# Optimization experiments

Measured on AMD Instinct MI355X. Metric: run time of the kernel, lower is better.

## Reference

```python
import jax, jax.numpy as jnp
import numpy as np

N_NODES = 100000
N_EDGES = 3200000
D_IN = 128
D_HID = 128
D_FF = 256
N_CLASSES = 26
N_GRAPHS = 512


def setup_inputs() -> dict:
    key = jax.random.key(0)
    ks = jax.random.split(key, 12)
    s = 0.05
    return {
        "x": jax.random.normal(ks[0], (N_NODES, D_IN), dtype=jnp.float32),
        "edge_index": jax.random.randint(ks[1], (2, N_EDGES), 0, N_NODES, dtype=jnp.int64),
        "batch": jnp.sort(jax.random.randint(ks[2], (N_NODES,), 0, N_GRAPHS, dtype=jnp.int64)),
        "W1": jax.random.normal(ks[3], (D_IN, D_HID), dtype=jnp.float32) * s,
        "b1": jnp.zeros((D_HID,), dtype=jnp.float32),
        "W2": jax.random.normal(ks[4], (D_HID, D_HID), dtype=jnp.float32) * s,
        "b2": jnp.zeros((D_HID,), dtype=jnp.float32),
        "W3": jax.random.normal(ks[5], (D_HID, D_HID), dtype=jnp.float32) * s,
        "b3": jnp.zeros((D_HID,), dtype=jnp.float32),
        "Wfc": jax.random.normal(ks[6], (D_HID, D_FF), dtype=jnp.float32) * s,
        "bfc": jnp.zeros((D_FF,), dtype=jnp.float32),
        "Wfc2": jax.random.normal(ks[7], (D_FF, N_CLASSES), dtype=jnp.float32) * s,
        "bfc2": jnp.zeros((N_CLASSES,), dtype=jnp.float32),
    }


def _gcn_layer(x, src, dst, norm, W, b):
    # GCNConv: h = x @ W; out[dst] += norm_e * h[src]; out += b
    h = x @ W                                   # [N, D]
    msg = h[src] * norm[:, None]                # [E+N, D] gather + scale
    agg = jax.ops.segment_sum(msg, dst, num_segments=N_NODES)
    return agg + b


def reference(x, edge_index, batch, W1, b1, W2, b2, W3, b3, Wfc, bfc, Wfc2, bfc2):
    # add self-loops (PyG GCNConv default) and compute symmetric normalization once
    loop = jnp.arange(N_NODES, dtype=edge_index.dtype)
    src = jnp.concatenate([edge_index[0], loop])
    dst = jnp.concatenate([edge_index[1], loop])
    deg = jax.ops.segment_sum(jnp.ones_like(dst, dtype=x.dtype), dst, num_segments=N_NODES)
    dinv = jnp.where(deg > 0, jax.lax.rsqrt(deg), 0.0)
    norm = dinv[src] * dinv[dst]               # D^{-1/2} A_hat D^{-1/2}

    h = jax.nn.relu(_gcn_layer(x, src, dst, norm, W1, b1))
    h = jax.nn.relu(_gcn_layer(h, src, dst, norm, W2, b2))
    h = jax.nn.relu(_gcn_layer(h, src, dst, norm, W3, b3))

    # global mean pool over graphs
    sums = jax.ops.segment_sum(h, batch, num_segments=N_GRAPHS)       # [G, D]
    cnts = jax.ops.segment_sum(jnp.ones((h.shape[0],), h.dtype), batch, num_segments=N_GRAPHS)
    pooled = sums / jnp.maximum(cnts, 1.0)[:, None]

    out = jax.nn.relu(pooled @ Wfc + bfc)       # dropout is identity at inference
    return out @ Wfc2 + bfc2                    # [G, num_classes]
```

## Files before the change

kernel.cpp:

```cpp
#include <hip/hip_runtime.h>
#include <hip/hip_bf16.h>

typedef __bf16 bf16;
typedef __attribute__((ext_vector_type(8))) __bf16 bf16x8;
typedef __attribute__((ext_vector_type(4))) float f32x4;

constexpr int N_NODES   = 100000;
constexpr int N_PAD     = 100032;
constexpr int D         = 128;
constexpr int D_FF      = 256;
constexpr int N_CLASSES = 26;
constexpr int N_GRAPHS  = 512;
constexpr int NB1       = 256;
constexpr int NBUCK     = (N_NODES + 511) / 512;

__device__ inline float2 bf2f(unsigned u) {
    float lo = __uint_as_float(u << 16);
    float hi = __uint_as_float(u & 0xffff0000u);
    return make_float2(lo, hi);
}


__global__ __launch_bounds__(1024) void p1_hist(const int* __restrict__ edst,
                                                int* __restrict__ gcount, int e) {
    __shared__ int cnt[NBUCK];
    for (int t = threadIdx.x; t < NBUCK; t += 1024) cnt[t] = 0;
    __syncthreads();
    int chunk = (e + NB1 - 1) / NB1;
    int lo = blockIdx.x * chunk;
    int hi = min(e, lo + chunk);
    for (int i = lo + threadIdx.x; i < hi; i += 1024)
        atomicAdd(&cnt[edst[i] >> 9], 1);
    __syncthreads();
    for (int t = threadIdx.x; t < NBUCK; t += 1024)
        gcount[t * NB1 + blockIdx.x] = cnt[t];
}

__global__ __launch_bounds__(256) void scan1(const int* __restrict__ in,
                                             int* out, int* bsum, int n) {
    __shared__ int sd[256];
    int i = blockIdx.x * 256 + threadIdx.x;
    int v = (i < n) ? in[i] : 0;
    sd[threadIdx.x] = v; __syncthreads();
    for (int off = 1; off < 256; off <<= 1) {
        int t = (threadIdx.x >= off) ? sd[threadIdx.x - off] : 0;
        __syncthreads();
        sd[threadIdx.x] += t;
        __syncthreads();
    }
    if (i < n) out[i] = sd[threadIdx.x] - v;
    if (threadIdx.x == 255) bsum[blockIdx.x] = sd[255];
}

__global__ __launch_bounds__(1024) void misc_kernel(const int* __restrict__ bsum,
                                                    int* __restrict__ boff, int nb,
                                                    const int* __restrict__ batch,
                                                    int* __restrict__ starts, int n,
                                                    const float* __restrict__ W0,
                                                    const float* __restrict__ W1,
                                                    const float* __restrict__ W2,
                                                    bf16* __restrict__ WT3) {
    int t = threadIdx.x;
    if (blockIdx.x == 0) {
        if (t <= N_GRAPHS) {
            int lo = 0, hi = n;
            while (lo < hi) {
                int mid = (lo + hi) >> 1;
                if (batch[mid] < t) lo = mid + 1; else hi = mid;
            }
            starts[t] = lo;
        }
        __shared__ int sd[1024];
        int v = (t < nb) ? bsum[t] : 0;
        sd[t] = v; __syncthreads();
        for (int off = 1; off < 1024; off <<= 1) {
            int x = (t >= off) ? sd[t - off] : 0;
            __syncthreads();
            sd[t] += x;
            __syncthreads();
        }
        if (t < nb) boff[t] = sd[t] - v;
    } else {
        int idx = (blockIdx.x - 1) * 1024 + t;
        int l = idx >> 14;
        int rem = idx & 16383;
        int nn = rem >> 7;
        int kk = rem & 127;
        const float* W = (l == 0) ? W0 : (l == 1) ? W1 : W2;
        WT3[idx] = (bf16)W[kk * D + nn];
    }
}

__global__ __launch_bounds__(1024) void p3_scatter(const int* __restrict__ esrc,
                                                   const int* __restrict__ edst,
                                                   const int* __restrict__ gbase,
                                                   const int* __restrict__ boff,
                                                   int* __restrict__ ebuf, int e) {
    __shared__ int cur[NBUCK];
    for (int t = threadIdx.x; t < NBUCK; t += 1024)
        cur[t] = gbase[t * NB1 + blockIdx.x] + boff[t];
    __syncthreads();
    int chunk = (e + NB1 - 1) / NB1;
    int lo = blockIdx.x * chunk;
    int hi = min(e, lo + chunk);
    for (int i = lo + threadIdx.x; i < hi; i += 1024) {
        int d = edst[i], s = esrc[i];
        int pos = atomicAdd(&cur[d >> 9], 1);
        ebuf[pos] = (s << 9) | (d & 511);
    }
}

__global__ __launch_bounds__(1024) void p45_fill(const int* __restrict__ ebuf,
                                                 const int* __restrict__ gbase,
                                                 const int* __restrict__ boff,
                                                 float* __restrict__ dinv,
                                                 int* __restrict__ rowptr,
                                                 int* __restrict__ csrc, int e, int n) {
    __shared__ int cnt[512];
    __shared__ int ps[512];
    __shared__ int cur[512];
    int b = blockIdx.x, t = threadIdx.x;
    if (t < 512) cnt[t] = 0;
    __syncthreads();
    int lo = gbase[b * NB1] + boff[b];
    int hi = (b + 1 < NBUCK) ? gbase[(b + 1) * NB1] + boff[b + 1] : e;
    for (int i = lo + t; i < hi; i += 1024)
        atomicAdd(&cnt[ebuf[i] & 511], 1);
    __syncthreads();
    int a = (t < 512) ? cnt[t] : 0;
    if (t < 512) ps[t] = a;
    __syncthreads();
    for (int off = 1; off < 512; off <<= 1) {
        int v = (t >= off && t < 512) ? ps[t - off] : 0;
        __syncthreads();
        if (t < 512) ps[t] += v;
        __syncthreads();
    }
    if (t < 512) {
        int g0 = lo + ps[t] - a;
        int node = b * 512 + t;
        cur[t] = g0;
        if (node < n) {
            rowptr[node] = g0;
            dinv[node] = 1.0f / sqrtf((float)(a + 1));
        }
    }
    if (b == 0 && t == 0) rowptr[n] = e;
    __syncthreads();
    for (int i = lo + t; i < hi; i += 1024) {
        int pe = ebuf[i];
        int pos = atomicAdd(&cur[pe & 511], 1);
        csrc[pos] = pe >> 9;
    }
}


__global__ __launch_bounds__(256) void gemm_kernel(const bf16* __restrict__ A,
                                                   const bf16* __restrict__ WT,
                                                   bf16* __restrict__ C,
                                                   const float* __restrict__ dinv, int n) {
    int wave = threadIdx.x >> 6;
    int lane = threadIdx.x & 63;
    int m16  = lane & 15;
    int quad = lane >> 4;
    int row0 = blockIdx.x * 64 + wave * 16;

    bf16x8 a[4];
    const bf16* arow = A + (row0 + m16) * D + quad * 8;
#pragma unroll
    for (int kt = 0; kt < 4; ++kt)
        a[kt] = *(const bf16x8*)(arow + kt * 32);

    float sc[4];
#pragma unroll
    for (int r = 0; r < 4; ++r) {
        int rr = row0 + quad * 4 + r;
        sc[r] = (rr < n) ? dinv[rr] : 0.f;
    }

#pragma unroll
    for (int nt = 0; nt < 8; ++nt) {
        f32x4 acc = {0.f, 0.f, 0.f, 0.f};
        const bf16* brow = WT + (nt * 16 + m16) * D + quad * 8;
#pragma unroll
        for (int kt = 0; kt < 4; ++kt) {
            bf16x8 b = *(const bf16x8*)(brow + kt * 32);
            acc = __builtin_amdgcn_mfma_f32_16x16x32_bf16(a[kt], b, acc, 0, 0, 0);
        }
#pragma unroll
        for (int r = 0; r < 4; ++r)
            C[(row0 + quad * 4 + r) * D + nt * 16 + m16] = (bf16)(sc[r] * acc[r]);
    }
}

__global__ __launch_bounds__(256) void gemm_f32_kernel(const float* __restrict__ A,
                                                       const bf16* __restrict__ WT,
                                                       bf16* __restrict__ C,
                                                       const float* __restrict__ dinv, int n) {
    int wave = threadIdx.x >> 6;
    int lane = threadIdx.x & 63;
    int m16  = lane & 15;
    int quad = lane >> 4;
    int row0 = blockIdx.x * 64 + wave * 16;
    int arowi = row0 + m16;

    bf16x8 a[4];
    const float* arow = A + (size_t)arowi * D + quad * 8;
#pragma unroll
    for (int kt = 0; kt < 4; ++kt) {
        float4 f0 = make_float4(0.f, 0.f, 0.f, 0.f);
        float4 f1 = make_float4(0.f, 0.f, 0.f, 0.f);
        if (arowi < n) {
            f0 = *(const float4*)(arow + kt * 32);
            f1 = *(const float4*)(arow + kt * 32 + 4);
        }
        bf16x8 v = { (bf16)f0.x, (bf16)f0.y, (bf16)f0.z, (bf16)f0.w,
                     (bf16)f1.x, (bf16)f1.y, (bf16)f1.z, (bf16)f1.w };
        a[kt] = v;
    }

    float sc[4];
#pragma unroll
    for (int r = 0; r < 4; ++r) {
        int rr = row0 + quad * 4 + r;
        sc[r] = (rr < n) ? dinv[rr] : 0.f;
    }

#pragma unroll
    for (int nt = 0; nt < 8; ++nt) {
        f32x4 acc = {0.f, 0.f, 0.f, 0.f};
        const bf16* brow = WT + (nt * 16 + m16) * D + quad * 8;
#pragma unroll
        for (int kt = 0; kt < 4; ++kt) {
            bf16x8 b = *(const bf16x8*)(brow + kt * 32);
            acc = __builtin_amdgcn_mfma_f32_16x16x32_bf16(a[kt], b, acc, 0, 0, 0);
        }
#pragma unroll
        for (int r = 0; r < 4; ++r)
            C[(row0 + quad * 4 + r) * D + nt * 16 + m16] = (bf16)(sc[r] * acc[r]);
    }
}

__global__ __launch_bounds__(256) void spmm_kernel(const bf16* __restrict__ h,
                                                   const int* __restrict__ rowptr,
                                                   const int* __restrict__ csrc,
                                                   const float* __restrict__ dinv,
                                                   const float* __restrict__ bias,
                                                   bf16* __restrict__ out, int n) {
    int v = blockIdx.x * 4 + (threadIdx.x >> 6);
    if (v >= n) return;
    int lane = threadIdx.x & 63;
    int g = lane >> 4;
    int c = lane & 15;
    int s = rowptr[v], e = rowptr[v + 1];
    float dv = dinv[v];

    float acc[8] = {0.f, 0.f, 0.f, 0.f, 0.f, 0.f, 0.f, 0.f};

    if (g == 0) {
        uint4 u = *(const uint4*)(h + (size_t)v * D + c * 8);
        float2 f0 = bf2f(u.x), f1 = bf2f(u.y), f2 = bf2f(u.z), f3 = bf2f(u.w);
        acc[0] = f0.x; acc[1] = f0.y; acc[2] = f1.x; acc[3] = f1.y;
        acc[4] = f2.x; acc[5] = f2.y; acc[6] = f3.x; acc[7] = f3.y;
    }

    int j = s + g;
    for (; j + 12 < e; j += 16) {
        int s0 = csrc[j], s1 = csrc[j + 4], s2 = csrc[j + 8], s3 = csrc[j + 12];
        uint4 u0 = *(const uint4*)(h + (size_t)s0 * D + c * 8);
        uint4 u1 = *(const uint4*)(h + (size_t)s1 * D + c * 8);
        uint4 u2 = *(const uint4*)(h + (size_t)s2 * D + c * 8);
        uint4 u3 = *(const uint4*)(h + (size_t)s3 * D + c * 8);
        {
            float2 a0 = bf2f(u0.x), a1 = bf2f(u0.y), a2 = bf2f(u0.z), a3 = bf2f(u0.w);
            acc[0] += a0.x; acc[1] += a0.y; acc[2] += a1.x; acc[3] += a1.y;
            acc[4] += a2.x; acc[5] += a2.y; acc[6] += a3.x; acc[7] += a3.y;
        }
        {
            float2 a0 = bf2f(u1.x), a1 = bf2f(u1.y), a2 = bf2f(u1.z), a3 = bf2f(u1.w);
            acc[0] += a0.x; acc[1] += a0.y; acc[2] += a1.x; acc[3] += a1.y;
            acc[4] += a2.x; acc[5] += a2.y; acc[6] += a3.x; acc[7] += a3.y;
        }
        {
            float2 a0 = bf2f(u2.x), a1 = bf2f(u2.y), a2 = bf2f(u2.z), a3 = bf2f(u2.w);
            acc[0] += a0.x; acc[1] += a0.y; acc[2] += a1.x; acc[3] += a1.y;
            acc[4] += a2.x; acc[5] += a2.y; acc[6] += a3.x; acc[7] += a3.y;
        }
        {
            float2 a0 = bf2f(u3.x), a1 = bf2f(u3.y), a2 = bf2f(u3.z), a3 = bf2f(u3.w);
            acc[0] += a0.x; acc[1] += a0.y; acc[2] += a1.x; acc[3] += a1.y;
            acc[4] += a2.x; acc[5] += a2.y; acc[6] += a3.x; acc[7] += a3.y;
        }
    }
    for (; j < e; j += 4) {
        int s0 = csrc[j];
        uint4 u0 = *(const uint4*)(h + (size_t)s0 * D + c * 8);
        float2 a0 = bf2f(u0.x), a1 = bf2f(u0.y), a2 = bf2f(u0.z), a3 = bf2f(u0.w);
        acc[0] += a0.x; acc[1] += a0.y; acc[2] += a1.x; acc[3] += a1.y;
        acc[4] += a2.x; acc[5] += a2.y; acc[6] += a3.x; acc[7] += a3.y;
    }

#pragma unroll
    for (int d = 0; d < 8; ++d) {
        acc[d] += __shfl_xor(acc[d], 16);
        acc[d] += __shfl_xor(acc[d], 32);
    }

    if (g == 0) {
        float4 bi0 = *(const float4*)(bias + c * 8);
        float4 bi1 = *(const float4*)(bias + c * 8 + 4);
        bf16x8 o;
        o[0] = (bf16)fmaxf(fmaf(dv, acc[0], bi0.x), 0.f);
        o[1] = (bf16)fmaxf(fmaf(dv, acc[1], bi0.y), 0.f);
        o[2] = (bf16)fmaxf(fmaf(dv, acc[2], bi0.z), 0.f);
        o[3] = (bf16)fmaxf(fmaf(dv, acc[3], bi0.w), 0.f);
        o[4] = (bf16)fmaxf(fmaf(dv, acc[4], bi1.x), 0.f);
        o[5] = (bf16)fmaxf(fmaf(dv, acc[5], bi1.y), 0.f);
        o[6] = (bf16)fmaxf(fmaf(dv, acc[6], bi1.z), 0.f);
        o[7] = (bf16)fmaxf(fmaf(dv, acc[7], bi1.w), 0.f);
        *(bf16x8*)(out + v * D + c * 8) = o;
    }
}

__global__ __launch_bounds__(256) void poolfc_kernel(const bf16* __restrict__ h,
                                                     const int* __restrict__ starts,
                                                     const float* __restrict__ Wfc,
                                                     const float* __restrict__ bfc,
                                                     const float* __restrict__ Wfc2,
                                                     const float* __restrict__ bfc2,
                                                     float* __restrict__ out) {
    __shared__ float part[3][D];
    __shared__ float pr[D];
    __shared__ float hid[D_FF];
    __shared__ float red[N_CLASSES][9];
    int g = blockIdx.x;
    int w = threadIdx.x >> 6, lane = threadIdx.x & 63;
    int s = starts[g], e = starts[g + 1];
    float ax = 0.f, ay = 0.f;
    for (int r = s + w; r < e; r += 4) {
        unsigned u = *(const unsigned*)(h + r * D + lane * 2);
        float2 f = bf2f(u);
        ax += f.x; ay += f.y;
    }
    if (w > 0) { part[w - 1][lane * 2] = ax; part[w - 1][lane * 2 + 1] = ay; }
    __syncthreads();
    if (w == 0) {
#pragma unroll
        for (int k = 0; k < 3; ++k) { ax += part[k][lane * 2]; ay += part[k][lane * 2 + 1]; }
        float c = fmaxf((float)(e - s), 1.0f);
        pr[lane * 2]     = ax / c;
        pr[lane * 2 + 1] = ay / c;
    }
    __syncthreads();
    int t = threadIdx.x;
    float a0 = 0.f, a1 = 0.f, a2 = 0.f, a3 = 0.f;
    for (int k = 0; k < D; k += 4) {
        a0 = fmaf(pr[k],     Wfc[k * D_FF + t],       a0);
        a1 = fmaf(pr[k + 1], Wfc[(k + 1) * D_FF + t], a1);
        a2 = fmaf(pr[k + 2], Wfc[(k + 2) * D_FF + t], a2);
        a3 = fmaf(pr[k + 3], Wfc[(k + 3) * D_FF + t], a3);
    }
    hid[t] = fmaxf((a0 + a1) + (a2 + a3) + bfc[t], 0.f);
    __syncthreads();
    if (t < N_CLASSES * 8) {
        int cls = t >> 3, kk = t & 7;
        float o = 0.f;
        for (int k = kk; k < D_FF; k += 8)
            o = fmaf(hid[k], Wfc2[k * N_CLASSES + cls], o);
        red[cls][kk] = o;
    }
    __syncthreads();
    if (t < N_CLASSES) {
        float o = bfc2[t];
#pragma unroll
        for (int k = 0; k < 8; ++k) o += red[t][k];
        out[g * N_CLASSES + t] = o;
    }
}


extern "C" void kernel_launch(void* const* d_in, const int* in_sizes, int n_in,
                              void* d_out, int out_size, void* d_ws, size_t ws_size,
                              hipStream_t stream) {
    const float* x     = (const float*)d_in[0];
    const int*   eidx  = (const int*)d_in[1];
    const int*   batch = (const int*)d_in[2];
    const float* W[3]  = { (const float*)d_in[3], (const float*)d_in[5], (const float*)d_in[7] };
    const float* b[3]  = { (const float*)d_in[4], (const float*)d_in[6], (const float*)d_in[8] };
    const float* Wfc   = (const float*)d_in[9];
    const float* bfc   = (const float*)d_in[10];
    const float* Wfc2  = (const float*)d_in[11];
    const float* bfc2  = (const float*)d_in[12];
    float* out = (float*)d_out;

    const int E = in_sizes[1] / 2;
    const int N = in_sizes[0] / D;
    const int* esrc = eidx;
    const int* edst = eidx + E;

    uint8_t* base = (uint8_t*)d_ws;
    size_t off = 0;
    auto alloc = [&](size_t bytes) -> void* {
        void* p = base + off;
        off = (off + bytes + 255) & ~(size_t)255;
        return p;
    };
    bf16*  hA     = (bf16*) alloc((size_t)N_PAD * D * 2);
    bf16*  hB     = (bf16*) alloc((size_t)N_PAD * D * 2);
    bf16*  WT3    = (bf16*) alloc((size_t)3 * D * D * 2);
    int*   csrc   = (int*)  alloc((size_t)E * 4);
    int*   ebuf   = (int*)  alloc((size_t)E * 4);
    int*   gcount = (int*)  alloc((size_t)NBUCK * NB1 * 4);
    int*   gbase  = (int*)  alloc((size_t)(NBUCK * NB1 + 1) * 4);
    int*   rowptr = (int*)  alloc((size_t)(N + 1) * 4);
    float* dinv   = (float*)alloc((size_t)N * 4);
    int*   bsum   = (int*)  alloc(4096);
    int*   boff   = (int*)  alloc(4096);
    int*   starts = (int*)  alloc((size_t)(N_GRAPHS + 1) * 4);
    (void)ws_size; (void)n_in; (void)out_size;

    const int GB  = N_PAD / 64;
    const int SB  = (N + 3) / 4;
    const int GCN = NBUCK * NB1;
    const int GCB = (GCN + 255) / 256;

    p1_hist<<<NB1, 1024, 0, stream>>>(edst, gcount, E);
    scan1<<<GCB, 256, 0, stream>>>(gcount, gbase, bsum, GCN);
    misc_kernel<<<49, 1024, 0, stream>>>(bsum, boff, GCB, batch, starts, N,
                                         W[0], W[1], W[2], WT3);
    p3_scatter<<<NB1, 1024, 0, stream>>>(esrc, edst, gbase, boff, ebuf, E);
    p45_fill<<<NBUCK, 1024, 0, stream>>>(ebuf, gbase, boff, dinv, rowptr, csrc, E, N);

    gemm_f32_kernel<<<GB, 256, 0, stream>>>(x, WT3, hA, dinv, N);
    spmm_kernel<<<SB, 256, 0, stream>>>(hA, rowptr, csrc, dinv, b[0], hB, N);
    for (int l = 1; l < 3; ++l) {
        gemm_kernel<<<GB, 256, 0, stream>>>(hB, WT3 + (size_t)l * D * D, hA, dinv, N);
        spmm_kernel<<<SB, 256, 0, stream>>>(hA, rowptr, csrc, dinv, b[l], hB, N);
    }

    poolfc_kernel<<<N_GRAPHS, 256, 0, stream>>>(hB, starts, Wfc, bfc, Wfc2, bfc2, out);
}
```

Baseline: 632.4 us.

## Fuse SpMM aggregation with next-layer GEMM through shared memory tile

```diff
diff --git a/kernel.cpp b/kernel.cpp
--- a/kernel.cpp
+++ b/kernel.cpp
@@ -155,44 +155,6 @@
 }
 
 
-__global__ __launch_bounds__(256) void gemm_kernel(const bf16* __restrict__ A,
-                                                   const bf16* __restrict__ WT,
-                                                   bf16* __restrict__ C,
-                                                   const float* __restrict__ dinv, int n) {
-    int wave = threadIdx.x >> 6;
-    int lane = threadIdx.x & 63;
-    int m16  = lane & 15;
-    int quad = lane >> 4;
-    int row0 = blockIdx.x * 64 + wave * 16;
-
-    bf16x8 a[4];
-    const bf16* arow = A + (row0 + m16) * D + quad * 8;
-#pragma unroll
-    for (int kt = 0; kt < 4; ++kt)
-        a[kt] = *(const bf16x8*)(arow + kt * 32);
-
-    float sc[4];
-#pragma unroll
-    for (int r = 0; r < 4; ++r) {
-        int rr = row0 + quad * 4 + r;
-        sc[r] = (rr < n) ? dinv[rr] : 0.f;
-    }
-
-#pragma unroll
-    for (int nt = 0; nt < 8; ++nt) {
-        f32x4 acc = {0.f, 0.f, 0.f, 0.f};
-        const bf16* brow = WT + (nt * 16 + m16) * D + quad * 8;
-#pragma unroll
-        for (int kt = 0; kt < 4; ++kt) {
-            bf16x8 b = *(const bf16x8*)(brow + kt * 32);
-            acc = __builtin_amdgcn_mfma_f32_16x16x32_bf16(a[kt], b, acc, 0, 0, 0);
-        }
-#pragma unroll
-        for (int r = 0; r < 4; ++r)
-            C[(row0 + quad * 4 + r) * D + nt * 16 + m16] = (bf16)(sc[r] * acc[r]);
-    }
-}
-
 __global__ __launch_bounds__(256) void gemm_f32_kernel(const float* __restrict__ A,
                                                        const bf16* __restrict__ WT,
                                                        bf16* __restrict__ C,
@@ -241,32 +203,25 @@
     }
 }
 
-__global__ __launch_bounds__(256) void spmm_kernel(const bf16* __restrict__ h,
-                                                   const int* __restrict__ rowptr,
-                                                   const int* __restrict__ csrc,
-                                                   const float* __restrict__ dinv,
-                                                   const float* __restrict__ bias,
-                                                   bf16* __restrict__ out, int n) {
-    int v = blockIdx.x * 4 + (threadIdx.x >> 6);
-    if (v >= n) return;
-    int lane = threadIdx.x & 63;
-    int g = lane >> 4;
-    int c = lane & 15;
-    int s = rowptr[v], e = rowptr[v + 1];
-    float dv = dinv[v];
-
-    float acc[8] = {0.f, 0.f, 0.f, 0.f, 0.f, 0.f, 0.f, 0.f};
-
-    if (g == 0) {
+__device__ inline void agg_node(const bf16* __restrict__ h, int v, int n, int c,
+                                const int* __restrict__ rowptr,
+                                const int* __restrict__ csrc,
+                                const float* __restrict__ dinv,
+                                float& dv, float acc[8]) {
+    int s = 0, e = 0;
+    dv = 0.f;
+    if (v < n) { s = rowptr[v]; e = rowptr[v + 1]; dv = dinv[v]; }
+#pragma unroll
+    for (int d = 0; d < 8; ++d) acc[d] = 0.f;
+    if (v < n) {
         uint4 u = *(const uint4*)(h + (size_t)v * D + c * 8);
         float2 f0 = bf2f(u.x), f1 = bf2f(u.y), f2 = bf2f(u.z), f3 = bf2f(u.w);
         acc[0] = f0.x; acc[1] = f0.y; acc[2] = f1.x; acc[3] = f1.y;
         acc[4] = f2.x; acc[5] = f2.y; acc[6] = f3.x; acc[7] = f3.y;
     }
-
-    int j = s + g;
-    for (; j + 12 < e; j += 16) {
-        int s0 = csrc[j], s1 = csrc[j + 4], s2 = csrc[j + 8], s3 = csrc[j + 12];
+    int j = s;
+    for (; j + 3 < e; j += 4) {
+        int s0 = csrc[j], s1 = csrc[j + 1], s2 = csrc[j + 2], s3 = csrc[j + 3];
         uint4 u0 = *(const uint4*)(h + (size_t)s0 * D + c * 8);
         uint4 u1 = *(const uint4*)(h + (size_t)s1 * D + c * 8);
         uint4 u2 = *(const uint4*)(h + (size_t)s2 * D + c * 8);
@@ -292,34 +247,93 @@
             acc[4] += a2.x; acc[5] += a2.y; acc[6] += a3.x; acc[7] += a3.y;
         }
     }
-    for (; j < e; j += 4) {
+    for (; j < e; ++j) {
         int s0 = csrc[j];
         uint4 u0 = *(const uint4*)(h + (size_t)s0 * D + c * 8);
         float2 a0 = bf2f(u0.x), a1 = bf2f(u0.y), a2 = bf2f(u0.z), a3 = bf2f(u0.w);
         acc[0] += a0.x; acc[1] += a0.y; acc[2] += a1.x; acc[3] += a1.y;
         acc[4] += a2.x; acc[5] += a2.y; acc[6] += a3.x; acc[7] += a3.y;
     }
-
-#pragma unroll
-    for (int d = 0; d < 8; ++d) {
-        acc[d] += __shfl_xor(acc[d], 16);
-        acc[d] += __shfl_xor(acc[d], 32);
-    }
-
-    if (g == 0) {
-        float4 bi0 = *(const float4*)(bias + c * 8);
-        float4 bi1 = *(const float4*)(bias + c * 8 + 4);
-        bf16x8 o;
-        o[0] = (bf16)fmaxf(fmaf(dv, acc[0], bi0.x), 0.f);
-        o[1] = (bf16)fmaxf(fmaf(dv, acc[1], bi0.y), 0.f);
-        o[2] = (bf16)fmaxf(fmaf(dv, acc[2], bi0.z), 0.f);
-        o[3] = (bf16)fmaxf(fmaf(dv, acc[3], bi0.w), 0.f);
-        o[4] = (bf16)fmaxf(fmaf(dv, acc[4], bi1.x), 0.f);
-        o[5] = (bf16)fmaxf(fmaf(dv, acc[5], bi1.y), 0.f);
-        o[6] = (bf16)fmaxf(fmaf(dv, acc[6], bi1.z), 0.f);
-        o[7] = (bf16)fmaxf(fmaf(dv, acc[7], bi1.w), 0.f);
-        *(bf16x8*)(out + v * D + c * 8) = o;
-    }
+}
+
+__device__ inline bf16x8 relu_row(float dv, const float acc[8],
+                                  const float* __restrict__ bias, int c) {
+    float4 bi0 = *(const float4*)(bias + c * 8);
+    float4 bi1 = *(const float4*)(bias + c * 8 + 4);
+    bf16x8 o;
+    o[0] = (bf16)fmaxf(fmaf(dv, acc[0], bi0.x), 0.f);
+    o[1] = (bf16)fmaxf(fmaf(dv, acc[1], bi0.y), 0.f);
+    o[2] = (bf16)fmaxf(fmaf(dv, acc[2], bi0.z), 0.f);
+    o[3] = (bf16)fmaxf(fmaf(dv, acc[3], bi0.w), 0.f);
+    o[4] = (bf16)fmaxf(fmaf(dv, acc[4], bi1.x), 0.f);
+    o[5] = (bf16)fmaxf(fmaf(dv, acc[5], bi1.y), 0.f);
+    o[6] = (bf16)fmaxf(fmaf(dv, acc[6], bi1.z), 0.f);
+    o[7] = (bf16)fmaxf(fmaf(dv, acc[7], bi1.w), 0.f);
+    return o;
+}
+
+__global__ __launch_bounds__(256) void spmm_gemm_kernel(const bf16* __restrict__ h,
+                                                        const int* __restrict__ rowptr,
+                                                        const int* __restrict__ csrc,
+                                                        const float* __restrict__ dinv,
+                                                        const float* __restrict__ bias,
+                                                        const bf16* __restrict__ WT,
+                                                        bf16* __restrict__ C, int n) {
+    __shared__ bf16 tile[16][136];
+    int t = threadIdx.x;
+    int grp = t >> 4;
+    int c   = t & 15;
+    int v   = blockIdx.x * 16 + grp;
+    float dv, acc[8];
+    agg_node(h, v, n, c, rowptr, csrc, dinv, dv, acc);
+    *(bf16x8*)(&tile[grp][c * 8]) = relu_row(dv, acc, bias, c);
+    __syncthreads();
+
+    int wave = t >> 6, lane = t & 63;
+    int m16 = lane & 15, quad = lane >> 4;
+    bf16x8 a[4];
+#pragma unroll
+    for (int kt = 0; kt < 4; ++kt)
+        a[kt] = *(const bf16x8*)(&tile[m16][quad * 8 + kt * 32]);
+
+    int base = blockIdx.x * 16;
+    float sc[4];
+#pragma unroll
+    for (int r = 0; r < 4; ++r) {
+        int rr = base + quad * 4 + r;
+        sc[r] = (rr < n) ? dinv[rr] : 0.f;
+    }
+
+#pragma unroll
+    for (int nt2 = 0; nt2 < 2; ++nt2) {
+        int nt = wave * 2 + nt2;
+        f32x4 accq = {0.f, 0.f, 0.f, 0.f};
+        const bf16* brow = WT + (nt * 16 + m16) * D + quad * 8;
+#pragma unroll
+        for (int kt = 0; kt < 4; ++kt) {
+            bf16x8 b = *(const bf16x8*)(brow + kt * 32);
+            accq = __builtin_amdgcn_mfma_f32_16x16x32_bf16(a[kt], b, accq, 0, 0, 0);
+        }
+#pragma unroll
+        for (int r = 0; r < 4; ++r)
+            C[(size_t)(base + quad * 4 + r) * D + nt * 16 + m16] = (bf16)(sc[r] * accq[r]);
+    }
+}
+
+__global__ __launch_bounds__(256) void spmm2_kernel(const bf16* __restrict__ h,
+                                                    const int* __restrict__ rowptr,
+                                                    const int* __restrict__ csrc,
+                                                    const float* __restrict__ dinv,
+                                                    const float* __restrict__ bias,
+                                                    bf16* __restrict__ out, int n) {
+    int t = threadIdx.x;
+    int grp = t >> 4;
+    int c   = t & 15;
+    int v   = blockIdx.x * 16 + grp;
+    float dv, acc[8];
+    agg_node(h, v, n, c, rowptr, csrc, dinv, dv, acc);
+    if (v < n)
+        *(bf16x8*)(out + (size_t)v * D + c * 8) = relu_row(dv, acc, bias, c);
 }
 
 __global__ __launch_bounds__(256) void poolfc_kernel(const bf16* __restrict__ h,
@@ -420,7 +434,7 @@
     (void)ws_size; (void)n_in; (void)out_size;
 
     const int GB  = N_PAD / 64;
-    const int SB  = (N + 3) / 4;
+    const int SGB = N_PAD / 16;
     const int GCN = NBUCK * NB1;
     const int GCB = (GCN + 255) / 256;
 
@@ -432,11 +446,11 @@
     p45_fill<<<NBUCK, 1024, 0, stream>>>(ebuf, gbase, boff, dinv, rowptr, csrc, E, N);
 
     gemm_f32_kernel<<<GB, 256, 0, stream>>>(x, WT3, hA, dinv, N);
-    spmm_kernel<<<SB, 256, 0, stream>>>(hA, rowptr, csrc, dinv, b[0], hB, N);
-    for (int l = 1; l < 3; ++l) {
-        gemm_kernel<<<GB, 256, 0, stream>>>(hB, WT3 + (size_t)l * D * D, hA, dinv, N);
-        spmm_kernel<<<SB, 256, 0, stream>>>(hA, rowptr, csrc, dinv, b[l], hB, N);
-    }
+    spmm_gemm_kernel<<<SGB, 256, 0, stream>>>(hA, rowptr, csrc, dinv, b[0],
+                                              WT3 + (size_t)1 * D * D, hB, N);
+    spmm_gemm_kernel<<<SGB, 256, 0, stream>>>(hB, rowptr, csrc, dinv, b[1],
+                                              WT3 + (size_t)2 * D * D, hA, N);
+    spmm2_kernel<<<SGB, 256, 0, stream>>>(hA, rowptr, csrc, dinv, b[2], hB, N);
 
     poolfc_kernel<<<N_GRAPHS, 256, 0, stream>>>(hB, starts, Wfc, bfc, Wfc2, bfc2, out);
 }
```

Result: faster. 580.6 us (-8.2%).
